# Optimization experiments

Measured on AMD Instinct MI355X. Metric: run time of the kernel, lower is better.

## Reference

```python
import jax, jax.numpy as jnp
import numpy as np

N, C, DK, DV = 8192, 128, 64, 64


def setup_inputs() -> dict:
    key = jax.random.key(0)
    ks = jax.random.split(key, 7)
    x = jax.random.normal(ks[0], (N, C), dtype=jnp.float32)
    # kaiming_normal for weights (std = sqrt(2/fan_in)), torch-default uniform bias
    std = float(np.sqrt(2.0 / C))
    bb = float(1.0 / np.sqrt(C))
    Wq = jax.random.normal(ks[1], (DK, C), dtype=jnp.float32) * std
    Wk = jax.random.normal(ks[2], (DK, C), dtype=jnp.float32) * std
    Wv = jax.random.normal(ks[3], (DV, C), dtype=jnp.float32) * std
    bq = jax.random.uniform(ks[4], (DK,), dtype=jnp.float32, minval=-bb, maxval=bb)
    bk = jax.random.uniform(ks[5], (DK,), dtype=jnp.float32, minval=-bb, maxval=bb)
    bv = jax.random.uniform(ks[6], (DV,), dtype=jnp.float32, minval=-bb, maxval=bb)
    return {"polyline_feature": x, "Wq": Wq, "bq": bq, "Wk": Wk, "bk": bk, "Wv": Wv, "bv": bv}


def reference(polyline_feature, Wq, bq, Wk, bk, Wv, bv):
    x = polyline_feature
    Q = jax.nn.relu(x @ Wq.T + bq)  # [N, DK]
    K = jax.nn.relu(x @ Wk.T + bk)  # [N, DK]
    V = jax.nn.relu(x @ Wv.T + bv)  # [N, DV]
    scores = (Q @ K.T) / jnp.sqrt(jnp.asarray(K.shape[1], Q.dtype))  # [N, N]
    attn = jax.nn.softmax(scores, axis=1)
    return attn @ V + Q  # residual on Q (non-standard)
```

## Files before the change

### kernel.cpp

```cpp
#include <hip/hip_runtime.h>


typedef __attribute__((ext_vector_type(8))) __bf16 bf16x8;
typedef __attribute__((ext_vector_type(4))) float f32x4;
typedef __attribute__((ext_vector_type(16))) float f32x16;

constexpr int N_ROWS = 8192;
constexpr int CDIM   = 128;
constexpr int DKV    = 64;
constexpr int KVS    = 256;
constexpr float SCALE_Q = 0.125f * 1.4426950408889634f;

__device__ __forceinline__ float fast_exp2(float x) {
    return __builtin_amdgcn_exp2f(x);
}

__device__ __forceinline__ unsigned short f2bf(float x) {
    union { float f; unsigned u; } v; v.f = x;
    unsigned r = v.u + 0x7fffu + ((v.u >> 16) & 1u);
    return (unsigned short)(r >> 16);
}

__device__ __forceinline__ float bf2f(unsigned short h) {
    union { unsigned u; float f; } v; v.u = (unsigned)h << 16; return v.f;
}

union Frag {
    unsigned u32[4];
    unsigned short u16[8];
    bf16x8 b;
    f32x4 f;
};

__global__ __launch_bounds__(128) void qkv_kernel(
    const float* __restrict__ x,
    const float* __restrict__ Wq, const float* __restrict__ bq,
    const float* __restrict__ Wk, const float* __restrict__ bk,
    const float* __restrict__ Wv, const float* __restrict__ bv,
    unsigned short* __restrict__ Qb, unsigned short* __restrict__ Kb,
    unsigned short* __restrict__ Vt, float* __restrict__ Qf)
{
    const int tid = threadIdx.x;
    const int w  = tid >> 6;
    const int l  = tid & 63;
    const int g  = l >> 4;
    const int lm = l & 15;
    const int n_base = blockIdx.x * 32 + w * 16;

    bf16x8 af[4];
    {
        const float* xrow = x + (size_t)(n_base + lm) * CDIM;
        #pragma unroll
        for (int s = 0; s < 4; ++s) {
            f32x4 lo = *(const f32x4*)(xrow + s * 32 + g * 8);
            f32x4 hi = *(const f32x4*)(xrow + s * 32 + g * 8 + 4);
            Frag fr;
            #pragma unroll
            for (int j = 0; j < 4; ++j) { fr.u16[j] = f2bf(lo[j]); fr.u16[4 + j] = f2bf(hi[j]); }
            af[s] = fr.b;
        }
    }

    const float* Ws[3] = {Wq, Wk, Wv};
    const float* Bs[3] = {bq, bk, bv};
    #pragma unroll
    for (int mat = 0; mat < 3; ++mat) {
        #pragma unroll
        for (int ct = 0; ct < 4; ++ct) {
            const int f = ct * 16 + lm;
            const float* wrow = Ws[mat] + (size_t)f * CDIM;
            f32x4 acc = {0.f, 0.f, 0.f, 0.f};
            #pragma unroll
            for (int s = 0; s < 4; ++s) {
                f32x4 lo = *(const f32x4*)(wrow + s * 32 + g * 8);
                f32x4 hi = *(const f32x4*)(wrow + s * 32 + g * 8 + 4);
                Frag fr;
                #pragma unroll
                for (int j = 0; j < 4; ++j) { fr.u16[j] = f2bf(lo[j]); fr.u16[4 + j] = f2bf(hi[j]); }
                acc = __builtin_amdgcn_mfma_f32_16x16x32_bf16(af[s], fr.b, acc, 0, 0, 0);
            }
            const float bias = Bs[mat][f];
            #pragma unroll
            for (int j = 0; j < 4; ++j) {
                const int n = n_base + g * 4 + j;
                const float v = fmaxf(acc[j] + bias, 0.f);
                if (mat == 0) {
                    Qf[(size_t)n * DKV + f] = v;
                    Qb[(size_t)n * DKV + f] = f2bf(v * SCALE_Q);
                } else if (mat == 1) {
                    Kb[(size_t)n * DKV + f] = f2bf(v);
                } else {
                    Vt[(size_t)f * N_ROWS + n] = f2bf(v);
                }
            }
        }
    }
}

__global__ __launch_bounds__(512) void attn_kernel(
    const unsigned short* __restrict__ Qb, const unsigned short* __restrict__ Kb,
    const unsigned short* __restrict__ Vt,
    unsigned short* __restrict__ PartOb, float* __restrict__ PartL,
    int nchunk)
{
    __shared__ __align__(16) unsigned short K_lds[KVS * DKV];
    __shared__ __align__(16) unsigned short V_lds[DKV * KVS];

    const int tid = threadIdx.x;
    const int w  = tid >> 6;
    const int l  = tid & 63;
    const int c  = l & 31;
    const int hB = l >> 5;
    const int qb = blockIdx.x;
    const int sp = blockIdx.y;
    const int q0 = qb * 256 + w * 32;

    bf16x8 qf0, qf1, qf2, qf3;
    {
        const unsigned short* qp = Qb + (size_t)(q0 + c) * DKV + hB * 8;
        qf0 = *(const bf16x8*)(qp);
        qf1 = *(const bf16x8*)(qp + 16);
        qf2 = *(const bf16x8*)(qp + 32);
        qf3 = *(const bf16x8*)(qp + 48);
    }

    f32x16 o0 = {}, o1 = {};
    float lsum = 0.f;

    const int swzK = ((c & 7) ^ (((c >> 3) & 3) << 1)) << 4;

    for (int ch = 0; ch < nchunk; ++ch) {
        const int kv0 = (sp * nchunk + ch) * KVS;
        if (ch > 0) __syncthreads();

        #pragma unroll
        for (int i = 0; i < 4; ++i) {
            const int rk = w * 8 + (l >> 3) + 64 * i;
            const int sk = ((l & 7) ^ ((rk & 7) ^ (((rk >> 3) & 3) << 1))) * 8;
            __builtin_amdgcn_global_load_lds(
                (const __attribute__((address_space(1))) unsigned int*)(Kb + (size_t)(kv0 + rk) * DKV + sk),
                (__attribute__((address_space(3))) unsigned int*)&K_lds[i * 4096 + w * 512], 16, 0, 0);
            const int rv = w * 2 + (l >> 5) + 16 * i;
            const int sv = ((l & 31) ^ (rv & 31)) * 8;
            __builtin_amdgcn_global_load_lds(
                (const __attribute__((address_space(1))) unsigned int*)(Vt + (size_t)rv * N_ROWS + kv0 + sv),
                (__attribute__((address_space(3))) unsigned int*)&V_lds[i * 4096 + w * 512], 16, 0, 0);
        }
        __syncthreads();

        #pragma unroll 1
        for (int kt = 0; kt < 4; ++kt) {
            const char* Kl = (const char*)K_lds + (size_t)kt * 64 * 128;

            f32x16 st0 = {}, st1 = {};
            #pragma unroll
            for (int ks = 0; ks < 4; ++ks) {
                const int cb = ks * 32 + hB * 16;
                bf16x8 a0 = *(const bf16x8*)(Kl + c * 128 + (cb ^ swzK));
                bf16x8 a1 = *(const bf16x8*)(Kl + (32 + c) * 128 + (cb ^ swzK));
                const bf16x8 qv = (ks == 0) ? qf0 : (ks == 1) ? qf1 : (ks == 2) ? qf2 : qf3;
                st0 = __builtin_amdgcn_mfma_f32_32x32x16_bf16(a0, qv, st0, 0, 0, 0);
                st1 = __builtin_amdgcn_mfma_f32_32x32x16_bf16(a1, qv, st1, 0, 0, 0);
            }

            unsigned pk[16];
            float ls = 0.f;
            #pragma unroll
            for (int p = 0; p < 8; ++p) {
                float a = fast_exp2(st0[2 * p]);
                float b = fast_exp2(st0[2 * p + 1]);
                ls += a + b;
                union { unsigned u; __bf16 h[2]; } uu;
                uu.h[0] = (__bf16)a; uu.h[1] = (__bf16)b;
                pk[p] = uu.u;
            }
            #pragma unroll
            for (int p = 0; p < 8; ++p) {
                float a = fast_exp2(st1[2 * p]);
                float b = fast_exp2(st1[2 * p + 1]);
                ls += a + b;
                union { unsigned u; __bf16 h[2]; } uu;
                uu.h[0] = (__bf16)a; uu.h[1] = (__bf16)b;
                pk[8 + p] = uu.u;
            }
            lsum += ls;

            #pragma unroll
            for (int ks = 0; ks < 4; ++ks) {
                const int base = (ks >> 1) * 8 + (ks & 1) * 4;
                const unsigned ownA  = hB ? pk[base + 2] : pk[base + 0];
                const unsigned ownB  = hB ? pk[base + 3] : pk[base + 1];
                const unsigned contA = hB ? pk[base + 0] : pk[base + 2];
                const unsigned contB = hB ? pk[base + 1] : pk[base + 3];
                const unsigned crossA = __shfl_xor(contA, 32);
                const unsigned crossB = __shfl_xor(contB, 32);
                Frag pf;
                pf.u32[0] = hB ? crossA : ownA;
                pf.u32[1] = hB ? crossB : ownB;
                pf.u32[2] = hB ? ownA : crossA;
                pf.u32[3] = hB ? ownB : crossB;
                const int sl = (kt * 8 + ks * 2 + hB) ^ c;
                bf16x8 v0 = *(const bf16x8*)((const char*)V_lds + c * 512 + sl * 16);
                bf16x8 v1 = *(const bf16x8*)((const char*)V_lds + (32 + c) * 512 + sl * 16);
                o0 = __builtin_amdgcn_mfma_f32_32x32x16_bf16(v0, pf.b, o0, 0, 0, 0);
                o1 = __builtin_amdgcn_mfma_f32_32x32x16_bf16(v1, pf.b, o1, 0, 0, 0);
            }
        }
    }

    lsum += __shfl_xor(lsum, 32);

    {
        unsigned short* po = PartOb + ((size_t)sp * N_ROWS + q0 + c) * 64;
        #pragma unroll
        for (int rq = 0; rq < 4; ++rq) {
            union { unsigned u[2]; __bf16 h[4]; } pa, pb;
            #pragma unroll
            for (int j = 0; j < 4; ++j) { pa.h[j] = (__bf16)o0[4 * rq + j]; pb.h[j] = (__bf16)o1[4 * rq + j]; }
            *(uint2*)(po + 8 * rq + 4 * hB)      = *(uint2*)pa.u;
            *(uint2*)(po + 32 + 8 * rq + 4 * hB) = *(uint2*)pb.u;
        }
    }
    if (hB == 0)
        PartL[(size_t)sp * N_ROWS + q0 + c] = lsum;
}

__global__ __launch_bounds__(256) void merge_kernel(
    const unsigned short* __restrict__ PartOb, const float* __restrict__ PartL,
    const float* __restrict__ Qf, float* __restrict__ out, int split)
{
    const int gid = blockIdx.x * 256 + threadIdx.x;
    const int q  = gid >> 5;
    const int dp = gid & 31;

    float L = 0.f, a0 = 0.f, a1 = 0.f;
    for (int s = 0; s < split; ++s) {
        L += PartL[(size_t)s * N_ROWS + q];
        const unsigned v = *(const unsigned*)(PartOb + ((size_t)s * N_ROWS + q) * 64 + 2 * dp);
        a0 += bf2f((unsigned short)(v & 0xffffu));
        a1 += bf2f((unsigned short)(v >> 16));
    }
    const float invL = 1.f / L;
    const int d0 = 2 * dp;
    out[(size_t)q * 64 + d0]     = a0 * invL + Qf[(size_t)q * 64 + d0];
    out[(size_t)q * 64 + d0 + 1] = a1 * invL + Qf[(size_t)q * 64 + d0 + 1];
}

extern "C" void kernel_launch(void* const* d_in, const int* in_sizes, int n_in,
                              void* d_out, int out_size, void* d_ws, size_t ws_size,
                              hipStream_t stream)
{
    const float* x  = (const float*)d_in[0];
    const float* Wq = (const float*)d_in[1];
    const float* bq = (const float*)d_in[2];
    const float* Wk = (const float*)d_in[3];
    const float* bk = (const float*)d_in[4];
    const float* Wv = (const float*)d_in[5];
    const float* bv = (const float*)d_in[6];
    float* out = (float*)d_out;

    char* ws = (char*)d_ws;
    size_t off = 0;
    auto take = [&](size_t bytes) {
        char* p = ws + off;
        off += (bytes + 255) & ~(size_t)255;
        return p;
    };
    unsigned short* Qb = (unsigned short*)take((size_t)N_ROWS * DKV * 2);
    unsigned short* Kb = (unsigned short*)take((size_t)N_ROWS * DKV * 2);
    unsigned short* Vt = (unsigned short*)take((size_t)DKV * N_ROWS * 2);
    float*          Qf = (float*)take((size_t)N_ROWS * DKV * 4);

    int split = 32, nchunk = 1;
    const size_t per_split = (size_t)N_ROWS * 64 * 2 + (size_t)N_ROWS * 4 + 512;
    while (split > 1 && off + (size_t)split * per_split > ws_size) { split >>= 1; nchunk <<= 1; }

    unsigned short* PartOb = (unsigned short*)take((size_t)split * N_ROWS * 64 * 2);
    float*          PartL  = (float*)take((size_t)split * N_ROWS * 4);

    qkv_kernel<<<dim3(N_ROWS / 32), dim3(128), 0, stream>>>(
        x, Wq, bq, Wk, bk, Wv, bv, Qb, Kb, Vt, Qf);
    attn_kernel<<<dim3(N_ROWS / 256, split), dim3(512), 0, stream>>>(
        Qb, Kb, Vt, PartOb, PartL, nchunk);
    merge_kernel<<<dim3(N_ROWS * 32 / 256), dim3(256), 0, stream>>>(
        PartOb, PartL, Qf, out, split);
}
```

Measured before the change: 58.28 us.

## Software-pipeline QK^T MFMAs with exp/PV work and halve KV split count

Restructures the inner kv-tile loop so the next tile's K fragments are loaded from LDS and its QK^T MFMAs are issued while the current tile's exp2/softmax and PV MFMAs run. Score accumulators are double-buffered and the loop is fully unrolled. The KV split count drops from 32 to 16 with two chunks per block, which cuts partial-output traffic and merge work but halves grid parallelism. The extra live accumulators raise register pressure and could lower occupancy.

```diff
diff --git a/kernel.cpp b/kernel.cpp
--- a/kernel.cpp
+++ b/kernel.cpp
@@ -129,6 +129,30 @@
 
     const int swzK = ((c & 7) ^ (((c >> 3) & 3) << 1)) << 4;
 
+    f32x16 sA[2], sB[2];
+    bf16x8 kfr0[4], kfr1[4];
+
+#define LDK(KT) do { \
+    const char* Kp_ = (const char*)K_lds + (size_t)(KT) * 64 * 128; \
+    _Pragma("unroll") \
+    for (int ks = 0; ks < 4; ++ks) { \
+        const int cb_ = ks * 32 + hB * 16; \
+        kfr0[ks] = *(const bf16x8*)(Kp_ + c * 128 + (cb_ ^ swzK)); \
+        kfr1[ks] = *(const bf16x8*)(Kp_ + (32 + c) * 128 + (cb_ ^ swzK)); \
+    } \
+} while (0)
+
+#define QKSTEP(P) do { \
+    f32x16 z_ = {}; \
+    sA[P] = z_; sB[P] = z_; \
+    _Pragma("unroll") \
+    for (int ks = 0; ks < 4; ++ks) { \
+        const bf16x8 qv_ = (ks == 0) ? qf0 : (ks == 1) ? qf1 : (ks == 2) ? qf2 : qf3; \
+        sA[P] = __builtin_amdgcn_mfma_f32_32x32x16_bf16(kfr0[ks], qv_, sA[P], 0, 0, 0); \
+        sB[P] = __builtin_amdgcn_mfma_f32_32x32x16_bf16(kfr1[ks], qv_, sB[P], 0, 0, 0); \
+    } \
+} while (0)
+
     for (int ch = 0; ch < nchunk; ++ch) {
         const int kv0 = (sp * nchunk + ch) * KVS;
         if (ch > 0) __syncthreads();
@@ -148,27 +172,22 @@
         }
         __syncthreads();
 
-        #pragma unroll 1
+        LDK(0);
+        QKSTEP(0);
+
+        #pragma unroll
         for (int kt = 0; kt < 4; ++kt) {
-            const char* Kl = (const char*)K_lds + (size_t)kt * 64 * 128;
-
-            f32x16 st0 = {}, st1 = {};
-            #pragma unroll
-            for (int ks = 0; ks < 4; ++ks) {
-                const int cb = ks * 32 + hB * 16;
-                bf16x8 a0 = *(const bf16x8*)(Kl + c * 128 + (cb ^ swzK));
-                bf16x8 a1 = *(const bf16x8*)(Kl + (32 + c) * 128 + (cb ^ swzK));
-                const bf16x8 qv = (ks == 0) ? qf0 : (ks == 1) ? qf1 : (ks == 2) ? qf2 : qf3;
-                st0 = __builtin_amdgcn_mfma_f32_32x32x16_bf16(a0, qv, st0, 0, 0, 0);
-                st1 = __builtin_amdgcn_mfma_f32_32x32x16_bf16(a1, qv, st1, 0, 0, 0);
-            }
+            const int P  = kt & 1;
+            const int PN = (kt + 1) & 1;
+
+            if (kt < 3) LDK(kt + 1);
 
             unsigned pk[16];
             float ls = 0.f;
             #pragma unroll
             for (int p = 0; p < 8; ++p) {
-                float a = fast_exp2(st0[2 * p]);
-                float b = fast_exp2(st0[2 * p + 1]);
+                float a = fast_exp2(sA[P][2 * p]);
+                float b = fast_exp2(sA[P][2 * p + 1]);
                 ls += a + b;
                 union { unsigned u; __bf16 h[2]; } uu;
                 uu.h[0] = (__bf16)a; uu.h[1] = (__bf16)b;
@@ -176,14 +195,16 @@
             }
             #pragma unroll
             for (int p = 0; p < 8; ++p) {
-                float a = fast_exp2(st1[2 * p]);
-                float b = fast_exp2(st1[2 * p + 1]);
+                float a = fast_exp2(sB[P][2 * p]);
+                float b = fast_exp2(sB[P][2 * p + 1]);
                 ls += a + b;
                 union { unsigned u; __bf16 h[2]; } uu;
                 uu.h[0] = (__bf16)a; uu.h[1] = (__bf16)b;
                 pk[8 + p] = uu.u;
             }
             lsum += ls;
+
+            if (kt < 3) QKSTEP(PN);
 
             #pragma unroll
             for (int ks = 0; ks < 4; ++ks) {
@@ -207,6 +228,8 @@
             }
         }
     }
+#undef LDK
+#undef QKSTEP
 
     lsum += __shfl_xor(lsum, 32);
 
@@ -271,7 +294,7 @@
     unsigned short* Vt = (unsigned short*)take((size_t)DKV * N_ROWS * 2);
     float*          Qf = (float*)take((size_t)N_ROWS * DKV * 4);
 
-    int split = 32, nchunk = 1;
+    int split = 16, nchunk = 2;
     const size_t per_split = (size_t)N_ROWS * 64 * 2 + (size_t)N_ROWS * 4 + 512;
     while (split > 1 && off + (size_t)split * per_split > ws_size) { split >>= 1; nchunk <<= 1; }
 
```

Result: slower. 67.64 us (+16.1%).
